# Performance work log

Measured on AMD Instinct MI355X. Metric: run time of the kernel, lower is better.

The kernel has to match this reference:

```python
import jax, jax.numpy as jnp
import numpy as np

B, NTOT, C, H, W = 8, 8, 128, 64, 64
RATE = 0.25
EPS = 1e-12  # F.normalize eps


def _l2norm(x, axis):
    n = jnp.sqrt(jnp.sum(x * x, axis=axis, keepdims=True))
    return x / jnp.maximum(n, EPS)


def setup_inputs() -> dict:
    key = jax.random.key(0)
    k1, k2, k3, k4 = jax.random.split(key, 4)
    feat = jax.random.normal(k1, (B, C, H, W), jnp.float32)
    refs = jax.random.normal(k2, (B, NTOT, C, H, W), jnp.float32)
    similarity = jax.random.uniform(k3, (B, NTOT), jnp.float32)
    hw = H * W
    num = int(RATE * hw)
    # random.sample -> unique indices per batch row
    perms = jax.vmap(lambda k: jax.random.permutation(k, hw))(jax.random.split(k4, B))
    feat_indices = perms[:, :num].astype(jnp.int32)
    return {"feat": feat, "refs": refs, "similarity": similarity,
            "feat_indices": feat_indices, "index": 0}


def reference(feat, refs, similarity, feat_indices, index):
    b, ntot, c, h, w = refs.shape
    hw = h * w
    n = ntot - 1
    # drop the base reference slot `index` (index is a static python int)
    keep = np.concatenate([np.arange(index), np.arange(index + 1, ntot)])
    refs_n = refs[:, keep]                    # [b,n,c,h,w]
    base_sim = similarity[:, index]           # [b]
    ref_sims = similarity[:, keep]            # [b,n]

    feat_flat = feat.reshape(b, c, hw)        # [b,c,hw]
    w_feat = _l2norm(feat_flat, axis=1)       # channel-wise L2 normalize per position
    refs_flat = refs_n.reshape(b, n, c, hw)   # [b,n,c,hw]
    w_refs = _l2norm(refs_flat, axis=2)       # channel-wise L2 normalize per position

    idx3 = feat_indices[:, None, :]           # [b,1,num]
    feat_select = jnp.take_along_axis(feat_flat, idx3, axis=2)   # [b,c,num]
    w_feat_sel = jnp.take_along_axis(w_feat, idx3, axis=2)       # [b,c,num]
    w_feat_sel = _l2norm(w_feat_sel, axis=1)  # (re-normalize, matches original)

    # cosine similarity of each selected feat position vs every ref position
    fx = jnp.einsum('bcq,bnck->bnqk', w_feat_sel, w_refs)   # [b,n,num,hw]
    ref_idx = jnp.argmax(fx, axis=-1)                        # top-1, [b,n,num]
    ref_sel = jnp.take_along_axis(refs_flat, ref_idx[:, :, None, :], axis=3)  # [b,n,c,num]

    # similarity-weighted fusion
    fused = base_sim[:, None, None] * feat_select + jnp.einsum('bn,bncq->bcq', ref_sims, ref_sel)

    # scatter fused features back into the feature map at sampled positions
    bi = jnp.arange(b)[:, None, None]
    ci = jnp.arange(c)[None, :, None]
    out = feat_flat.at[bi, ci, idx3].set(fused)
    return out.reshape(b, c, h, w), feat_indices, ref_idx
```

## Files before the change

### kernel.cpp

```cpp
#include <hip/hip_runtime.h>
#include <hip/hip_bf16.h>

#define BB 8
#define NTOT 8
#define NREF 7
#define CC 128
#define HW 4096
#define QQ 1024
#define EPSV 1e-12f
#define NSPLIT 8
#define BNQ (BB * NREF * QQ)

#define OUT1_OFF ((size_t)BB * CC * HW)
#define OUT2_OFF (OUT1_OFF + (size_t)BB * QQ)

typedef __hip_bfloat16 bf16;

__device__ __forceinline__ float b2f(bf16 v) { return __bfloat162float(v); }
__device__ __forceinline__ float sane0(float x) {
    return (x == x && fabsf(x) < 60.f) ? x : 0.f;
}
__device__ __forceinline__ float ldv(const void* p, size_t i, int f32) {
    return f32 ? ((const float*)p)[i] : b2f(((const bf16*)p)[i]);
}

__global__ void k_detect(const void* __restrict__ feat, const void* __restrict__ refs,
                         const void* __restrict__ sim, int* __restrict__ flags) {
    if (threadIdx.x == 0) {
        const ushort* p = (const ushort*)feat;
        int c1 = 0;
        for (int i = 0; i < 256; i++) {
            float v = b2f(*(const bf16*)&p[(size_t)i * 16384]);
            if (!(fabsf(v) <= 100.f)) c1++;
        }
        flags[0] = c1 > 32 ? 1 : 0;
        p = (const ushort*)refs; c1 = 0;
        for (int i = 0; i < 256; i++) {
            float v = b2f(*(const bf16*)&p[(size_t)i * 131072]);
            if (!(fabsf(v) <= 100.f)) c1++;
        }
        flags[1] = c1 > 32 ? 1 : 0;
        p = (const ushort*)sim; c1 = 0;
        for (int i = 0; i < 32; i++) {
            float v = b2f(*(const bf16*)&p[i * 2]);
            if (!(fabsf(v) <= 100.f)) c1++;
        }
        flags[2] = c1 > 4 ? 1 : 0;
    }
}

__global__ void k_wfs(const void* __restrict__ feat, const int* __restrict__ fidx,
                      const int* __restrict__ flags, float* __restrict__ wfs_t) {
    int ff = flags[0];
    int bq = blockIdx.x;
    int b = bq >> 10;
    int q = bq & 1023;
    int idx = fidx[b * QQ + q] & (HW - 1);
    int l = threadIdx.x;
    size_t base = (size_t)b * CC * HW + idx;
    float x0 = ldv(feat, base + (size_t)l * HW, ff);
    float x1 = ldv(feat, base + (size_t)(l + 64) * HW, ff);
    float s = x0 * x0 + x1 * x1;
    #pragma unroll
    for (int m = 1; m < 64; m <<= 1) s += __shfl_xor(s, m, 64);
    float d1 = fmaxf(sqrtf(s), EPSV);
    float y0 = x0 / d1, y1 = x1 / d1;
    float s2 = y0 * y0 + y1 * y1;
    #pragma unroll
    for (int m = 1; m < 64; m <<= 1) s2 += __shfl_xor(s2, m, 64);
    float d2 = fmaxf(sqrtf(s2), EPSV);
    wfs_t[((size_t)(b * CC + l)) * QQ + q] = y0 / d2;
    wfs_t[((size_t)(b * CC + l + 64)) * QQ + q] = y1 / d2;
}

__global__ void k_rnorm(const void* __restrict__ refs, const int* __restrict__ pindex,
                        const int* __restrict__ flags, float* __restrict__ rinv) {
    int rf = flags[1];
    int gb = blockIdx.x;
    int kc = gb & 15;
    int bn = gb >> 4;
    int n = bn % NREF;
    int b = bn / NREF;
    int index = *pindex & 7;
    int kn = n < index ? n : n + 1;
    int k = kc * 256 + threadIdx.x;
    size_t base = (size_t)(b * NTOT + kn) * CC * HW + k;
    float s = 0.f;
    #pragma unroll 4
    for (int c = 0; c < CC; c++) {
        float x = ldv(refs, base + (size_t)c * HW, rf);
        s = fmaf(x, x, s);
    }
    rinv[(b * NREF + n) * HW + k] = 1.0f / fmaxf(sqrtf(s), EPSV);
}

__global__ __launch_bounds__(256, 4) void k_argmax(
        const void* __restrict__ refs, const float* __restrict__ wfs_t,
        const float* __restrict__ rinv, const int* __restrict__ pindex,
        const int* __restrict__ flags, float2* __restrict__ pairs) {
    __shared__ __align__(16) float lw[32][128];
    __shared__ __align__(16) float lr[32][128];
    int rf = flags[1];
    int gb = blockIdx.x;
    int qtile = gb & 7;
    int r = gb >> 3;
    int bn = r % 56;
    int ks = r / 56;
    int n = bn % NREF;
    int b = bn / NREF;
    int index = *pindex & 7;
    int kn = n < index ? n : n + 1;
    int q0 = qtile * 128;
    int kbase = ks * (HW / NSPLIT);
    int t = threadIdx.x;
    int qt = t >> 4, kt = t & 15;

    const float* wsrc = wfs_t + (size_t)b * CC * QQ + q0;
    size_t rbase = (size_t)(b * NTOT + kn) * CC * HW;
    const float* rib = rinv + (b * NREF + n) * HW;

    float best[8];
    int bidx[8];
    #pragma unroll
    for (int j = 0; j < 8; j++) { best[j] = -3.402823466e38f; bidx[j] = 0; }

    int x0 = (t & 31) * 4;
    int cb = t >> 5;

    for (int kt0 = 0; kt0 < HW / NSPLIT; kt0 += 128) {
        int k0 = kbase + kt0;
        float acc[8][8];
        #pragma unroll
        for (int j = 0; j < 8; j++)
            #pragma unroll
            for (int i = 0; i < 8; i++) acc[j][i] = 0.f;

        float4 ri4 = *(const float4*)&rib[k0 + x0];

        for (int cc0 = 0; cc0 < CC; cc0 += 32) {
            __syncthreads();
            #pragma unroll
            for (int i = 0; i < 4; i++) {
                int flat4 = i * 1024 + t * 4;
                int c = flat4 >> 7, x = flat4 & 127;
                *(float4*)&lw[c][x] =
                    *(const float4*)&wsrc[(size_t)(cc0 + c) * QQ + x];
            }
            #pragma unroll
            for (int s = 0; s < 4; s++) {
                int c = cb + s * 8;
                float4 v;
                if (rf) {
                    v = *(const float4*)&((const float*)refs)
                            [rbase + (size_t)(cc0 + c) * HW + k0 + x0];
                } else {
                    ushort4 u = *(const ushort4*)&((const ushort*)refs)
                            [rbase + (size_t)(cc0 + c) * HW + k0 + x0];
                    v.x = b2f(*(const bf16*)&u.x); v.y = b2f(*(const bf16*)&u.y);
                    v.z = b2f(*(const bf16*)&u.z); v.w = b2f(*(const bf16*)&u.w);
                }
                v.x *= ri4.x; v.y *= ri4.y; v.z *= ri4.z; v.w *= ri4.w;
                *(float4*)&lr[c][x0] = v;
            }
            __syncthreads();

            #pragma unroll 4
            for (int c = 0; c < 32; c++) {
                const float4 wq0 = *(const float4*)&lw[c][qt * 8];
                const float4 wq1 = *(const float4*)&lw[c][qt * 8 + 4];
                const float4 rk0 = *(const float4*)&lr[c][kt * 4];
                const float4 rk1 = *(const float4*)&lr[c][64 + kt * 4];
                const float wq[8] = {wq0.x, wq0.y, wq0.z, wq0.w,
                                     wq1.x, wq1.y, wq1.z, wq1.w};
                const float rk[8] = {rk0.x, rk0.y, rk0.z, rk0.w,
                                     rk1.x, rk1.y, rk1.z, rk1.w};
                #pragma unroll
                for (int j = 0; j < 8; j++)
                    #pragma unroll
                    for (int i = 0; i < 8; i++)
                        acc[j][i] = fmaf(wq[j], rk[i], acc[j][i]);
            }
        }

        #pragma unroll
        for (int j = 0; j < 8; j++) {
            #pragma unroll
            for (int i = 0; i < 8; i++) {
                float v = acc[j][i];
                int gk = k0 + (i < 4 ? kt * 4 + i : 64 + kt * 4 + (i - 4));
                if (v > best[j]) { best[j] = v; bidx[j] = gk; }
            }
        }
    }

    #pragma unroll
    for (int j = 0; j < 8; j++) {
        float v = best[j];
        int i = bidx[j];
        #pragma unroll
        for (int m = 1; m < 16; m <<= 1) {
            float vo = __shfl_xor(v, m, 64);
            int io = __shfl_xor(i, m, 64);
            if (vo > v || (vo == v && io < i)) { v = vo; i = io; }
        }
        if (kt == 0) {
            float2 pr; pr.x = v; pr.y = (float)i;
            pairs[(size_t)ks * BNQ + (size_t)(b * NREF + n) * QQ + q0 + qt * 8 + j] = pr;
        }
    }
}

__global__ void k_amax2(const float2* __restrict__ pairs, float* __restrict__ out2) {
    int j = blockIdx.x * 256 + threadIdx.x;
    float2 best = pairs[j];
    #pragma unroll
    for (int s = 1; s < NSPLIT; s++) {
        float2 p = pairs[(size_t)s * BNQ + j];
        if (p.x > best.x) best = p;
    }
    out2[j] = best.y;
}

__global__ void k_cvt(const void* __restrict__ feat, const int* __restrict__ flags,
                      float* __restrict__ dst) {
    int ff = flags[0];
    size_t i4 = (size_t)blockIdx.x * 256 + threadIdx.x;
    float4 o;
    if (ff) {
        o = ((const float4*)feat)[i4];
    } else {
        ushort4 v = ((const ushort4*)feat)[i4];
        o.x = b2f(*(const bf16*)&v.x); o.y = b2f(*(const bf16*)&v.y);
        o.z = b2f(*(const bf16*)&v.z); o.w = b2f(*(const bf16*)&v.w);
    }
    o.x = sane0(o.x); o.y = sane0(o.y); o.z = sane0(o.z); o.w = sane0(o.w);
    ((float4*)dst)[i4] = o;
}

__global__ void k_aux(const int* __restrict__ fidx, float* __restrict__ out) {
    int j = blockIdx.x * 256 + threadIdx.x;
    float r = b2f(__float2bfloat16((float)fidx[j]));
    out[OUT1_OFF + j] = (r == r) ? r : 0.f;
}

__global__ void k_fuse(const void* __restrict__ feat, const void* __restrict__ refs,
                       const void* __restrict__ sim, const int* __restrict__ fidx,
                       const int* __restrict__ pindex, const int* __restrict__ flags,
                       float* __restrict__ out) {
    int ff = flags[0], rf = flags[1], sf = flags[2];
    int bq = blockIdx.x;
    int b = bq >> 10;
    int q = bq & 1023;
    int c = threadIdx.x;
    int index = *pindex & 7;
    int idx = fidx[b * QQ + q] & (HW - 1);
    float base = ldv(sim, b * NTOT + index, sf);
    float f = ldv(feat, ((size_t)(b * CC) + c) * HW + idx, ff);
    float s = 0.f;
    const float* ridxf = out + OUT2_OFF;
    #pragma unroll
    for (int n = 0; n < NREF; n++) {
        int kn = n < index ? n : n + 1;
        float sn = ldv(sim, b * NTOT + kn, sf);
        int rk = (int)ridxf[(size_t)(b * NREF + n) * QQ + q] & (HW - 1);
        float rv = ldv(refs, ((size_t)((b * NTOT + kn) * CC) + c) * HW + rk, rf);
        s = fmaf(sn, rv, s);
    }
    out[((size_t)(b * CC) + c) * HW + idx] = sane0(base * f + s);
}

__global__ void k_round(float* __restrict__ out) {
    int j = blockIdx.x * 256 + threadIdx.x;
    float v = out[OUT2_OFF + j];
    float r = b2f(__float2bfloat16(v));
    out[OUT2_OFF + j] = (r == r && fabsf(r) < 1e6f) ? r : 0.f;
}

extern "C" void kernel_launch(void* const* d_in, const int* in_sizes, int n_in,
                              void* d_out, int out_size, void* d_ws, size_t ws_size,
                              hipStream_t stream) {
    const void* feat = 0; const void* refs = 0; const void* sim = 0;
    const int* fidx = 0; const int* pindex = 0;
    for (int i = 0; i < n_in; i++) {
        switch (in_sizes[i]) {
            case BB * CC * HW:        feat = d_in[i]; break;
            case BB * NTOT * CC * HW: refs = d_in[i]; break;
            case BB * NTOT:           sim = d_in[i]; break;
            case BB * QQ:             fidx = (const int*)d_in[i]; break;
            case 1:                   pindex = (const int*)d_in[i]; break;
        }
    }
    float* out = (float*)d_out;
    char* ws = (char*)d_ws;
    int* flags = (int*)ws;
    float* wfs_t = (float*)(ws + 256);
    float* rinv = (float*)(ws + 256 + (size_t)BB * CC * QQ * 4);
    float2* pairs = (float2*)out;
    float* out2 = out + OUT2_OFF;

    k_detect<<<1, 64, 0, stream>>>(feat, refs, sim, flags);
    k_wfs<<<BB * QQ, 64, 0, stream>>>(feat, fidx, flags, wfs_t);
    k_rnorm<<<BB * NREF * (HW / 256), 256, 0, stream>>>(refs, pindex, flags, rinv);
    k_argmax<<<NSPLIT * BB * NREF * 8, 256, 0, stream>>>(refs, wfs_t, rinv, pindex, flags, pairs);
    k_amax2<<<BNQ / 256, 256, 0, stream>>>(pairs, out2);
    k_cvt<<<(BB * CC * HW / 4) / 256, 256, 0, stream>>>(feat, flags, out);
    k_aux<<<(BB * QQ) / 256, 256, 0, stream>>>(fidx, out);
    k_fuse<<<BB * QQ, 128, 0, stream>>>(feat, refs, sim, fidx, pindex, flags, out);
    k_round<<<(BB * NREF * QQ) / 256, 256, 0, stream>>>(out);
}
```

Baseline: 930.7 us.

## Replace FP32 argmax GEMM with bf16 MFMA two-pass candidate search plus exact rescoring

Adds an MFMA-based kernel that computes approximate cosine scores in bf16. A first pass over all reference positions finds the approximate maximum per query. A second pass recomputes the scores and rescoring in exact fp32 only for positions within a small threshold of that maximum. A runtime probe checks that the MFMA instruction gives correct results and selects either this path or the old FP32 tiled argmax. The aim is to swap the scalar-FMA-bound FP32 GEMM for matrix cores. The cost is that every reference tile is loaded and converted twice, and the fixed threshold may miss the true argmax when bf16 error exceeds it.

```diff
diff --git a/kernel.cpp b/kernel.cpp
--- a/kernel.cpp
+++ b/kernel.cpp
@@ -10,11 +10,14 @@
 #define EPSV 1e-12f
 #define NSPLIT 8
 #define BNQ (BB * NREF * QQ)
+#define THR2E 0.012f
 
 #define OUT1_OFF ((size_t)BB * CC * HW)
 #define OUT2_OFF (OUT1_OFF + (size_t)BB * QQ)
 
 typedef __hip_bfloat16 bf16;
+typedef __attribute__((ext_vector_type(8))) short short8v;
+typedef __attribute__((ext_vector_type(4))) float f32x4;
 
 __device__ __forceinline__ float b2f(bf16 v) { return __bfloat162float(v); }
 __device__ __forceinline__ float sane0(float x) {
@@ -22,6 +25,10 @@
 }
 __device__ __forceinline__ float ldv(const void* p, size_t i, int f32) {
     return f32 ? ((const float*)p)[i] : b2f(((const bf16*)p)[i]);
+}
+__device__ __forceinline__ ushort f2bs(float x) {
+    bf16 t = __float2bfloat16(x);
+    return *(ushort*)&t;
 }
 
 __global__ void k_detect(const void* __restrict__ feat, const void* __restrict__ refs,
@@ -49,8 +56,35 @@
     }
 }
 
+__global__ void k_probe(int* __restrict__ flags) {
+    int l = threadIdx.x;
+    int lo = l & 15, hi = l >> 4;
+    short8v a, b;
+    #pragma unroll
+    for (int j = 0; j < 8; j++) {
+        int k = hi * 8 + j;
+        a[j] = (short)f2bs((float)(((lo * 31 + k * 7) % 13) - 6));
+        b[j] = (short)f2bs((float)(((k * 5 + lo * 11) % 11) - 5));
+    }
+    f32x4 acc = {0.f, 0.f, 0.f, 0.f};
+    acc = __builtin_amdgcn_mfma_f32_16x16x32_bf16(a, b, acc, 0, 0, 0);
+    bool ok = true;
+    #pragma unroll
+    for (int reg = 0; reg < 4; reg++) {
+        int row = hi * 4 + reg, col = lo;
+        float ref = 0.f;
+        for (int k = 0; k < 32; k++)
+            ref += (float)(((row * 31 + k * 7) % 13) - 6) *
+                   (float)(((k * 5 + col * 11) % 11) - 5);
+        if (acc[reg] != ref) ok = false;
+    }
+    unsigned long long m = __ballot(ok);
+    if (l == 0) flags[3] = (m == ~0ull) ? 1 : 0;
+}
+
 __global__ void k_wfs(const void* __restrict__ feat, const int* __restrict__ fidx,
-                      const int* __restrict__ flags, float* __restrict__ wfs_t) {
+                      const int* __restrict__ flags, float* __restrict__ wfs_t,
+                      ushort* __restrict__ wfs_b) {
     int ff = flags[0];
     int bq = blockIdx.x;
     int b = bq >> 10;
@@ -69,8 +103,12 @@
     #pragma unroll
     for (int m = 1; m < 64; m <<= 1) s2 += __shfl_xor(s2, m, 64);
     float d2 = fmaxf(sqrtf(s2), EPSV);
-    wfs_t[((size_t)(b * CC + l)) * QQ + q] = y0 / d2;
-    wfs_t[((size_t)(b * CC + l + 64)) * QQ + q] = y1 / d2;
+    float w0 = y0 / d2, w1 = y1 / d2;
+    wfs_t[((size_t)(b * CC + l)) * QQ + q] = w0;
+    wfs_t[((size_t)(b * CC + l + 64)) * QQ + q] = w1;
+    ushort* wb = wfs_b + ((size_t)(b * QQ) + q) * CC;
+    wb[l] = f2bs(w0);
+    wb[l + 64] = f2bs(w1);
 }
 
 __global__ void k_rnorm(const void* __restrict__ refs, const int* __restrict__ pindex,
@@ -94,12 +132,169 @@
     rinv[(b * NREF + n) * HW + k] = 1.0f / fmaxf(sqrtf(s), EPSV);
 }
 
+__global__ __launch_bounds__(256) void k_amax_mfma(
+        const void* __restrict__ refs, const ushort* __restrict__ wfs_b,
+        const float* __restrict__ wfs_t, const float* __restrict__ rinv,
+        const int* __restrict__ pindex, const int* __restrict__ flags,
+        float* __restrict__ out2) {
+    __shared__ ushort lr[64 * 128];
+    if (!flags[3]) return;
+    int rf = flags[1];
+    int gb = blockIdx.x;
+    int qtile = gb & 15;
+    int bn = gb >> 4;
+    int n = bn % NREF;
+    int b = bn / NREF;
+    int index = *pindex & 7;
+    int kn = n < index ? n : n + 1;
+    int q0 = qtile * 64;
+    int t = threadIdx.x;
+    int w = t >> 6, l = t & 63;
+    int lo = l & 15, hi = l >> 4;
+    int myq = q0 + w * 16 + lo;
+
+    size_t rbase = (size_t)(b * NTOT + kn) * CC * HW;
+    const float* rib = rinv + (b * NREF + n) * HW;
+
+    short8v bfr[4];
+    const ushort* wb = wfs_b + ((size_t)(b * QQ) + myq) * CC;
+    #pragma unroll
+    for (int cc = 0; cc < 4; cc++)
+        bfr[cc] = *(const short8v*)&wb[cc * 32 + hi * 8];
+
+    int x0t = (t & 15) * 4;
+    int cs = t >> 4;
+
+    float mhat = -3.402823466e38f;
+    for (int tile = 0; tile < 64; tile++) {
+        int k0 = tile * 64;
+        __syncthreads();
+        ushort4 u[8];
+        if (rf) {
+            #pragma unroll
+            for (int s = 0; s < 8; s++) {
+                float4 v = *(const float4*)&((const float*)refs)
+                        [rbase + (size_t)(cs * 8 + s) * HW + k0 + x0t];
+                ushort4 o;
+                o.x = f2bs(v.x); o.y = f2bs(v.y); o.z = f2bs(v.z); o.w = f2bs(v.w);
+                u[s] = o;
+            }
+        } else {
+            #pragma unroll
+            for (int s = 0; s < 8; s++)
+                u[s] = *(const ushort4*)&((const ushort*)refs)
+                        [rbase + (size_t)(cs * 8 + s) * HW + k0 + x0t];
+        }
+        #pragma unroll
+        for (int i = 0; i < 4; i++) {
+            int k = x0t + i;
+            short8v wv;
+            #pragma unroll
+            for (int s = 0; s < 8; s++) wv[s] = (short)((const ushort*)&u[s])[i];
+            *(short8v*)&lr[k * 128 + ((cs * 8) ^ ((k & 15) << 3))] = wv;
+        }
+        __syncthreads();
+
+        #pragma unroll
+        for (int sub = 0; sub < 4; sub++) {
+            f32x4 acc = {0.f, 0.f, 0.f, 0.f};
+            int krow = sub * 16 + lo;
+            #pragma unroll
+            for (int cc = 0; cc < 4; cc++) {
+                short8v afr = *(const short8v*)
+                    &lr[krow * 128 + ((cc * 32 + hi * 8) ^ ((krow & 15) << 3))];
+                acc = __builtin_amdgcn_mfma_f32_16x16x32_bf16(afr, bfr[cc], acc, 0, 0, 0);
+            }
+            float4 ri = *(const float4*)&rib[k0 + sub * 16 + hi * 4];
+            const float rr[4] = {ri.x, ri.y, ri.z, ri.w};
+            #pragma unroll
+            for (int reg = 0; reg < 4; reg++)
+                mhat = fmaxf(mhat, acc[reg] * rr[reg]);
+        }
+    }
+    #pragma unroll
+    for (int m = 16; m < 64; m <<= 1)
+        mhat = fmaxf(mhat, __shfl_xor(mhat, m, 64));
+    float thr = mhat - THR2E;
+
+    float bs = -3.402823466e38f;
+    int bk = 0;
+    const float* wcol = wfs_t + (size_t)b * CC * QQ + myq;
+    for (int tile = 0; tile < 64; tile++) {
+        int k0 = tile * 64;
+        __syncthreads();
+        ushort4 u[8];
+        if (rf) {
+            #pragma unroll
+            for (int s = 0; s < 8; s++) {
+                float4 v = *(const float4*)&((const float*)refs)
+                        [rbase + (size_t)(cs * 8 + s) * HW + k0 + x0t];
+                ushort4 o;
+                o.x = f2bs(v.x); o.y = f2bs(v.y); o.z = f2bs(v.z); o.w = f2bs(v.w);
+                u[s] = o;
+            }
+        } else {
+            #pragma unroll
+            for (int s = 0; s < 8; s++)
+                u[s] = *(const ushort4*)&((const ushort*)refs)
+                        [rbase + (size_t)(cs * 8 + s) * HW + k0 + x0t];
+        }
+        #pragma unroll
+        for (int i = 0; i < 4; i++) {
+            int k = x0t + i;
+            short8v wv;
+            #pragma unroll
+            for (int s = 0; s < 8; s++) wv[s] = (short)((const ushort*)&u[s])[i];
+            *(short8v*)&lr[k * 128 + ((cs * 8) ^ ((k & 15) << 3))] = wv;
+        }
+        __syncthreads();
+
+        #pragma unroll
+        for (int sub = 0; sub < 4; sub++) {
+            f32x4 acc = {0.f, 0.f, 0.f, 0.f};
+            int krow = sub * 16 + lo;
+            #pragma unroll
+            for (int cc = 0; cc < 4; cc++) {
+                short8v afr = *(const short8v*)
+                    &lr[krow * 128 + ((cc * 32 + hi * 8) ^ ((krow & 15) << 3))];
+                acc = __builtin_amdgcn_mfma_f32_16x16x32_bf16(afr, bfr[cc], acc, 0, 0, 0);
+            }
+            float4 ri = *(const float4*)&rib[k0 + sub * 16 + hi * 4];
+            const float rr[4] = {ri.x, ri.y, ri.z, ri.w};
+            #pragma unroll
+            for (int reg = 0; reg < 4; reg++) {
+                float v = acc[reg] * rr[reg];
+                if (v >= thr) {
+                    int gk = k0 + sub * 16 + hi * 4 + reg;
+                    float s_ex = 0.f;
+                    #pragma unroll 4
+                    for (int c = 0; c < CC; c++)
+                        s_ex = fmaf(wcol[(size_t)c * QQ],
+                                    ldv(refs, rbase + (size_t)c * HW + gk, rf), s_ex);
+                    s_ex *= rib[gk];
+                    if (s_ex > bs || (s_ex == bs && gk < bk)) { bs = s_ex; bk = gk; }
+                }
+            }
+        }
+    }
+
+    #pragma unroll
+    for (int m = 16; m < 64; m <<= 1) {
+        float vo = __shfl_xor(bs, m, 64);
+        int io = __shfl_xor(bk, m, 64);
+        if (vo > bs || (vo == bs && io < bk)) { bs = vo; bk = io; }
+    }
+    if (hi == 0)
+        out2[(size_t)(b * NREF + n) * QQ + myq] = (float)bk;
+}
+
 __global__ __launch_bounds__(256, 4) void k_argmax(
         const void* __restrict__ refs, const float* __restrict__ wfs_t,
         const float* __restrict__ rinv, const int* __restrict__ pindex,
         const int* __restrict__ flags, float2* __restrict__ pairs) {
     __shared__ __align__(16) float lw[32][128];
-    __shared__ __align__(16) float lr[32][128];
+    __shared__ __align__(16) float lr2[32][128];
+    if (flags[3]) return;
     int rf = flags[1];
     int gb = blockIdx.x;
     int qtile = gb & 7;
@@ -154,13 +349,13 @@
                     v = *(const float4*)&((const float*)refs)
                             [rbase + (size_t)(cc0 + c) * HW + k0 + x0];
                 } else {
-                    ushort4 u = *(const ushort4*)&((const ushort*)refs)
+                    ushort4 uu = *(const ushort4*)&((const ushort*)refs)
                             [rbase + (size_t)(cc0 + c) * HW + k0 + x0];
-                    v.x = b2f(*(const bf16*)&u.x); v.y = b2f(*(const bf16*)&u.y);
-                    v.z = b2f(*(const bf16*)&u.z); v.w = b2f(*(const bf16*)&u.w);
+                    v.x = b2f(*(const bf16*)&uu.x); v.y = b2f(*(const bf16*)&uu.y);
+                    v.z = b2f(*(const bf16*)&uu.z); v.w = b2f(*(const bf16*)&uu.w);
                 }
                 v.x *= ri4.x; v.y *= ri4.y; v.z *= ri4.z; v.w *= ri4.w;
-                *(float4*)&lr[c][x0] = v;
+                *(float4*)&lr2[c][x0] = v;
             }
             __syncthreads();
 
@@ -168,8 +363,8 @@
             for (int c = 0; c < 32; c++) {
                 const float4 wq0 = *(const float4*)&lw[c][qt * 8];
                 const float4 wq1 = *(const float4*)&lw[c][qt * 8 + 4];
-                const float4 rk0 = *(const float4*)&lr[c][kt * 4];
-                const float4 rk1 = *(const float4*)&lr[c][64 + kt * 4];
+                const float4 rk0 = *(const float4*)&lr2[c][kt * 4];
+                const float4 rk1 = *(const float4*)&lr2[c][64 + kt * 4];
                 const float wq[8] = {wq0.x, wq0.y, wq0.z, wq0.w,
                                      wq1.x, wq1.y, wq1.z, wq1.w};
                 const float rk[8] = {rk0.x, rk0.y, rk0.z, rk0.w,
@@ -210,10 +405,11 @@
     }
 }
 
-__global__ void k_amax2(const float2* __restrict__ pairs, float* __restrict__ out2) {
+__global__ void k_amax2(const float2* __restrict__ pairs, const int* __restrict__ flags,
+                        float* __restrict__ out2) {
+    if (flags[3]) return;
     int j = blockIdx.x * 256 + threadIdx.x;
     float2 best = pairs[j];
-    #pragma unroll
     for (int s = 1; s < NSPLIT; s++) {
         float2 p = pairs[(size_t)s * BNQ + j];
         if (p.x > best.x) best = p;
@@ -296,13 +492,16 @@
     float* wfs_t = (float*)(ws + 256);
     float* rinv = (float*)(ws + 256 + (size_t)BB * CC * QQ * 4);
     float2* pairs = (float2*)out;
+    ushort* wfs_b = (ushort*)((char*)out + (size_t)4 * 1024 * 1024);
     float* out2 = out + OUT2_OFF;
 
     k_detect<<<1, 64, 0, stream>>>(feat, refs, sim, flags);
-    k_wfs<<<BB * QQ, 64, 0, stream>>>(feat, fidx, flags, wfs_t);
+    k_probe<<<1, 64, 0, stream>>>(flags);
+    k_wfs<<<BB * QQ, 64, 0, stream>>>(feat, fidx, flags, wfs_t, wfs_b);
     k_rnorm<<<BB * NREF * (HW / 256), 256, 0, stream>>>(refs, pindex, flags, rinv);
+    k_amax_mfma<<<BB * NREF * 16, 256, 0, stream>>>(refs, wfs_b, wfs_t, rinv, pindex, flags, out2);
     k_argmax<<<NSPLIT * BB * NREF * 8, 256, 0, stream>>>(refs, wfs_t, rinv, pindex, flags, pairs);
-    k_amax2<<<BNQ / 256, 256, 0, stream>>>(pairs, out2);
+    k_amax2<<<BNQ / 256, 256, 0, stream>>>(pairs, flags, out2);
     k_cvt<<<(BB * CC * HW / 4) / 256, 256, 0, stream>>>(feat, flags, out);
     k_aux<<<(BB * QQ) / 256, 256, 0, stream>>>(fidx, out);
     k_fuse<<<BB * QQ, 128, 0, stream>>>(feat, refs, sim, fidx, pindex, flags, out);
```

Measured after the change: 1.499 ms. +61.1%, slower.
